# Optimization experiments

Measured on AMD Instinct MI355X. Metric: run time of the kernel, lower is better.

The kernel has to match this reference:

```python
import jax, jax.numpy as jnp
import numpy as np
import math

HIDDEN = 2048
HEADS = 16
HEAD_DIM = HIDDEN // HEADS
MAX_SEQ = 4096
ROPE_BASE = 10000.0


def rope_cos_sin(seq_len):
    # (seq_len, head_dim//2) angle table
    inv_freq = 1.0 / (ROPE_BASE ** (jnp.arange(0, HEAD_DIM, 2, dtype=jnp.float32) / HEAD_DIM))
    t = jnp.arange(seq_len, dtype=jnp.float32)
    ang = jnp.einsum('s,f->sf', t, inv_freq)
    return jnp.cos(ang), jnp.sin(ang)


def apply_rope(x, cos, sin):
    # x: (b, s, h, d); interleaved complex pairs along last dim
    b, s, h, d = x.shape
    xr = x.reshape(b, s, h, d // 2, 2)
    x0, x1 = xr[..., 0], xr[..., 1]
    c = cos[:s][None, :, None, :]
    sn = sin[:s][None, :, None, :]
    o0 = x0 * c - x1 * sn
    o1 = x0 * sn + x1 * c
    return jnp.stack([o0, o1], axis=-1).reshape(b, s, h, d)


def setup_inputs() -> dict:
    key = jax.random.key(0)
    k1, k2, k3, k4, k5, k6 = jax.random.split(key, 6)
    B, SQ, SK = 2, 2048, 2048
    x = jax.random.normal(k1, (B, SQ, HIDDEN), dtype=jnp.float32)
    enc = jax.random.normal(k2, (B, SK, HIDDEN), dtype=jnp.float32)
    mask = jnp.ones((B, SK), dtype=jnp.int32)
    scale = 0.02
    Wq = jax.random.normal(k3, (HIDDEN, HIDDEN), dtype=jnp.float32) * scale
    Wk = jax.random.normal(k4, (HIDDEN, HIDDEN), dtype=jnp.float32) * scale
    Wv = jax.random.normal(k5, (HIDDEN, HIDDEN), dtype=jnp.float32) * scale
    Wo = jax.random.normal(k6, (HIDDEN, HIDDEN), dtype=jnp.float32) * scale
    return {"x": x, "encoder_output": enc, "encoder_attention_mask": mask,
            "Wq": Wq, "Wk": Wk, "Wv": Wv, "Wo": Wo}


def reference(x, encoder_output, encoder_attention_mask, Wq, Wk, Wv, Wo):
    B, SQ, _ = x.shape
    SK = encoder_output.shape[1]
    # nn.Linear(bias=False): y = x @ W^T
    q = (x @ Wq.T).reshape(B, SQ, HEADS, HEAD_DIM)
    k = (encoder_output @ Wk.T).reshape(B, SK, HEADS, HEAD_DIM)
    v = (encoder_output @ Wv.T).reshape(B, SK, HEADS, HEAD_DIM)
    cos, sin = rope_cos_sin(max(SQ, SK))
    q = apply_rope(q, cos, sin)
    k = apply_rope(k, cos, sin)
    scale = math.sqrt(HEAD_DIM)
    # (b, h, sq, sk) scores
    scores = jnp.einsum('bqhd,bkhd->bhqk', q, k) / scale
    mask = encoder_attention_mask[:, None, None, :]
    scores = jnp.where(mask == 0, -jnp.inf, scores)
    attn = jax.nn.softmax(scores, axis=-1)
    out = jnp.einsum('bhqk,bkhd->bqhd', attn, v).reshape(B, SQ, HIDDEN)
    return out @ Wo.T
```

## Files before the change

### kernel.cpp

```cpp
#include <hip/hip_runtime.h>
#include <stdint.h>


#define LOG2E 1.44269504088896340736f
#define INV2PI 0.15915494309189535f

typedef __attribute__((ext_vector_type(8))) short bf16x8;
typedef __attribute__((ext_vector_type(8))) uint16_t u16x8;
typedef __attribute__((ext_vector_type(4))) uint16_t u16x4;
typedef __attribute__((ext_vector_type(4))) float f32x4;

__device__ __forceinline__ uint16_t f2bf(float f) {
  union { float f; uint32_t i; } v; v.f = f;
  uint32_t x = v.i;
  return (uint16_t)((x + 0x7fffu + ((x >> 16) & 1u)) >> 16);
}
__device__ __forceinline__ uint32_t f_as_u(float f) { union { float f; uint32_t u; } v; v.f = f; return v.u; }
__device__ __forceinline__ float u_as_f(uint32_t u) { union { uint32_t u; float f; } v; v.u = u; return v.f; }
__device__ __forceinline__ void glds16(const void* g, void* l) {
  __builtin_amdgcn_global_load_lds((const __attribute__((address_space(1))) void*)g,
                                   (__attribute__((address_space(3))) void*)l, 16, 0, 0);
}

__global__ __launch_bounds__(256) void convert_f32_bf16(const float* __restrict__ in,
                                                        uint16_t* __restrict__ out) {
  const long i = ((long)blockIdx.x * 256 + threadIdx.x) * 8;
  const f32x4 a = *(const f32x4*)(in + i);
  const f32x4 b = *(const f32x4*)(in + i + 4);
  u16x8 o;
#pragma unroll
  for (int j = 0; j < 4; ++j) { o[j] = f2bf(a[j]); o[4 + j] = f2bf(b[j]); }
  *(u16x8*)(out + i) = o;
}

__global__ __launch_bounds__(256) void convert_w4(const float* __restrict__ Wq,
                                                  const float* __restrict__ Wk,
                                                  const float* __restrict__ Wv,
                                                  const float* __restrict__ Wo,
                                                  uint16_t* __restrict__ W4) {
  const int blk = blockIdx.x;
  const int sec = blk >> 11;
  const long off = ((long)(blk & 2047) * 256 + threadIdx.x) * 8;
  const float* src = (sec == 0) ? Wq : (sec == 1) ? Wk : (sec == 2) ? Wv : Wo;
  const f32x4 a = *(const f32x4*)(src + off);
  const f32x4 b = *(const f32x4*)(src + off + 4);
  u16x8 o;
#pragma unroll
  for (int j = 0; j < 4; ++j) { o[j] = f2bf(a[j]); o[4 + j] = f2bf(b[j]); }
  *(u16x8*)(W4 + (long)sec * 4194304 + off) = o;
}

__global__ __launch_bounds__(256) void mask_bias(const int* __restrict__ m,
                                                 float* __restrict__ bias) {
  const int i = blockIdx.x * 256 + threadIdx.x;
  bias[i] = m[i] ? 0.0f : -__builtin_inff();
}

#define EPI_QKV 0
#define EPI_F32 1

__device__ __forceinline__ void epi_rope_store(uint16_t* C, const f32x4& a, int rowbase,
                                               int c, float oscale) {
  const int f = (c >> 1) & 63;
  const float inv = __builtin_amdgcn_exp2f((float)f * (-13.287712379549449f / 64.0f));
  const float sgn = (c & 1) ? 1.0f : -1.0f;
#pragma unroll
  for (int r = 0; r < 4; ++r) {
    const float val = a[r];
    const float partner = __shfl_xor(val, 1);
    const int s = (rowbase + r) & 2047;
    const float rev = __builtin_amdgcn_fractf((float)s * inv * INV2PI);
    const float sn = __builtin_amdgcn_sinf(rev);
    const float cs = __builtin_amdgcn_cosf(rev);
    C[(long)(rowbase + r) * 2048 + c] = f2bf((val * cs + sgn * partner * sn) * oscale);
  }
}

template <int MODE>
__global__ __launch_bounds__(512, 2) void gemm256(const uint16_t* __restrict__ A0,
                                                  const uint16_t* __restrict__ A1,
                                                  const uint16_t* __restrict__ W,
                                                  void* __restrict__ C0v,
                                                  void* __restrict__ C1v,
                                                  void* __restrict__ C2v,
                                                  int M, int N, int K, float oscale) {
  __shared__ __align__(16) uint16_t As[2][2][8192];
  __shared__ __align__(16) uint16_t Bs[2][2][8192];
  const int tid = threadIdx.x;
  const int lane = tid & 63;
  const int w = tid >> 6;
  const int r16 = lane & 15, quad = lane >> 4;
  const int wm = w >> 2, wn = w & 3;

  const int nby = M >> 8;
  const int nwg = gridDim.x;
  const int wg = ((int)blockIdx.x & 7) * (nwg >> 3) + ((int)blockIdx.x >> 3);
  const int by = wg % nby, bx = wg / nby;
  const int m0 = by << 8, n0 = bx << 8;

  const uint16_t* A = (MODE == EPI_QKV && n0 >= 2048) ? A1 : A0;

  const int srow = 2 * w * 16 + (lane >> 2);
  const int ssl = (lane & 3) ^ ((srow >> 1) & 3);
  const uint16_t* Ag0 = A + (long)(m0 + srow) * K + ssl * 8;
  const uint16_t* Ag1 = Ag0 + (long)16 * K;
  const uint16_t* Bg0 = W + (long)(n0 + srow) * K + ssl * 8;
  const uint16_t* Bg1 = Bg0 + (long)16 * K;
  const int ldso = w << 10;

  const int sw = (r16 >> 1) & 3;
  const int aoff = (wm * 128 + r16) * 32 + ((quad ^ sw) << 3);
  const int boff = (wn * 64 + r16) * 32 + ((quad ^ sw) << 3);

  f32x4 acc[8][4] = {};
  bf16x8 af[4], bfr[4];

#define SCHED0() __builtin_amdgcn_sched_barrier(0)
#define G_STAGE_A(BUF, KK, T) do { \
    glds16(Ag0 + (long)(T) * 64 + (KK) * 32, &As[BUF][KK][ldso]); \
    glds16(Ag1 + (long)(T) * 64 + (KK) * 32, &As[BUF][KK][ldso + 512]); } while (0)
#define G_STAGE_B(BUF, KK, T) do { \
    glds16(Bg0 + (long)(T) * 64 + (KK) * 32, &Bs[BUF][KK][ldso]); \
    glds16(Bg1 + (long)(T) * 64 + (KK) * 32, &Bs[BUF][KK][ldso + 512]); } while (0)
#define LDS_B(BUF, KK) do { _Pragma("unroll") \
    for (int i = 0; i < 4; ++i) bfr[i] = *(const bf16x8*)&Bs[BUF][KK][boff + i * 512]; } while (0)
#define LDS_A(BUF, KK, MH) do { _Pragma("unroll") \
    for (int i = 0; i < 4; ++i) af[i] = *(const bf16x8*)&As[BUF][KK][aoff + ((MH) * 4 + i) * 512]; } while (0)
#define MFMA16(MH) do { __builtin_amdgcn_s_setprio(1); _Pragma("unroll") \
    for (int mi = 0; mi < 4; ++mi) { _Pragma("unroll") \
      for (int nt = 0; nt < 4; ++nt) \
        acc[(MH) * 4 + mi][nt] = __builtin_amdgcn_mfma_f32_16x16x32_bf16(af[mi], bfr[nt], acc[(MH) * 4 + mi][nt], 0, 0, 0); } \
    __builtin_amdgcn_s_setprio(0); } while (0)
#define VMBAR(NN) do { SCHED0(); \
    asm volatile("s_waitcnt vmcnt(" #NN ")" ::: "memory"); \
    __builtin_amdgcn_s_barrier(); \
    SCHED0(); } while (0)
#define TILE_ITER(T, BC, BN) do { \
    G_STAGE_A(BN, 0, (T) + 1); LDS_B(BC, 0); LDS_A(BC, 0, 0); MFMA16(0); \
    G_STAGE_B(BN, 0, (T) + 1); LDS_A(BC, 0, 1); MFMA16(1); \
    VMBAR(4); \
    G_STAGE_A(BN, 1, (T) + 1); LDS_B(BC, 1); LDS_A(BC, 1, 0); MFMA16(0); \
    G_STAGE_B(BN, 1, (T) + 1); LDS_A(BC, 1, 1); MFMA16(1); \
    VMBAR(4); } while (0)

  G_STAGE_A(0, 0, 0); G_STAGE_B(0, 0, 0); G_STAGE_A(0, 1, 0); G_STAGE_B(0, 1, 0);
  VMBAR(4);

  const int NT = K >> 6;
  int t = 0;
  for (; t + 2 < NT; t += 2) { TILE_ITER(t, 0, 1); TILE_ITER(t + 1, 1, 0); }
  TILE_ITER(t, 0, 1);

  LDS_B(1, 0); LDS_A(1, 0, 0); MFMA16(0);
  LDS_A(1, 0, 1); MFMA16(1);
  VMBAR(0);
  LDS_B(1, 1); LDS_A(1, 1, 0); MFMA16(0);
  LDS_A(1, 1, 1); MFMA16(1);

#undef SCHED0
#undef G_STAGE_A
#undef G_STAGE_B
#undef LDS_A
#undef LDS_B
#undef MFMA16
#undef VMBAR
#undef TILE_ITER

#pragma unroll
  for (int mt = 0; mt < 8; ++mt)
#pragma unroll
    for (int nt = 0; nt < 4; ++nt) {
      const int col = n0 + wn * 64 + nt * 16 + r16;
      const int rowbase = m0 + wm * 128 + mt * 16 + quad * 4;
      if constexpr (MODE == EPI_F32) {
        float* C = (float*)C0v;
#pragma unroll
        for (int r = 0; r < 4; ++r)
          C[(long)(rowbase + r) * N + col] = acc[mt][nt][r];
      } else {
        if (n0 < 2048) {
          epi_rope_store((uint16_t*)C0v, acc[mt][nt], rowbase, col, oscale);
        } else if (n0 < 4096) {
          epi_rope_store((uint16_t*)C1v, acc[mt][nt], rowbase, col - 2048, 1.0f);
        } else {
          uint16_t* Vt = (uint16_t*)C2v;
          const int c = col - 4096;
          const int h = c >> 7, d = c & 127;
          const int b = rowbase >> 11, s = rowbase & 2047;
          u16x4 pk;
#pragma unroll
          for (int r = 0; r < 4; ++r) pk[r] = f2bf(acc[mt][nt][r]);
          *(u16x4*)(Vt + (long)((b * 16 + h) * 128 + d) * 2048 + s) = pk;
        }
      }
    }
}

__global__ __launch_bounds__(256) void attn_kernel(const uint16_t* __restrict__ Q,
                                                   const uint16_t* __restrict__ K,
                                                   const uint16_t* __restrict__ Vt,
                                                   const float* __restrict__ bias,
                                                   uint16_t* __restrict__ O) {
  __shared__ __align__(16) uint16_t Ks[2][32 * 128];
  __shared__ __align__(16) uint16_t Vts[2][128 * 32];
  __shared__ __align__(16) uint16_t Ps[4][32 * 40];
  const int tid = threadIdx.x;
  const int lane = tid & 63;
  const int w = tid >> 6;
  const int r16 = lane & 15, quad = lane >> 4;
  const int h = blockIdx.y, b = blockIdx.z;
  const int qbase = blockIdx.x * 128 + w * 32;

  bf16x8 qf[2][4];
#pragma unroll
  for (int t = 0; t < 2; ++t) {
    const uint16_t* qb = Q + ((long)(b * 2048 + qbase + t * 16 + r16)) * 2048 + h * 128 + quad * 8;
#pragma unroll
    for (int c = 0; c < 4; ++c) qf[t][c] = *(const bf16x8*)(qb + c * 32);
  }
  f32x4 oacc[2][8] = {};
  float li[2][4] = {};

  uint16_t* PsW = &Ps[w][0];
  const float* brow = bias + b * 2048;

  const int key0[2] = {8 * w + quad, 8 * w + 4 + quad};
  const uint16_t* kg[2];
  const uint16_t* vg[2];
#pragma unroll
  for (int i = 0; i < 2; ++i) {
    kg[i] = K + ((long)(b * 2048 + key0[i])) * 2048 + h * 128 + 8 * (r16 ^ ((4 * i + quad) & 7));
    const int dim = 32 * w + 16 * i + (lane >> 2);
    vg[i] = Vt + ((long)((b * 16 + h) * 128 + dim)) * 2048 + 8 * ((lane & 3) ^ ((lane >> 2) & 3));
  }

#pragma unroll
  for (int i = 0; i < 2; ++i) {
    glds16(kg[i], &Ks[0][(2 * w + i) * 512]);
    glds16(vg[i], &Vts[0][(2 * w + i) * 512]);
    kg[i] += 32 * 2048;
    vg[i] += 32;
  }
  float bn0 = brow[r16], bn1 = brow[16 + r16];

  auto body = [&](int k0, const uint16_t* Kc, const uint16_t* Vc,
                  uint16_t* Kn, uint16_t* Vn, bool pf) {
    __syncthreads();
    const float bc0 = bn0, bc1 = bn1;
    if (pf) {
#pragma unroll
      for (int i = 0; i < 2; ++i) {
        glds16(kg[i], Kn + (2 * w + i) * 512);
        glds16(vg[i], Vn + (2 * w + i) * 512);
        kg[i] += 32 * 2048;
        vg[i] += 32;
      }
      bn0 = brow[k0 + 32 + r16];
      bn1 = brow[k0 + 48 + r16];
    }
#pragma unroll
    for (int ct = 0; ct < 2; ++ct) {
      const int key = ct * 16 + r16;
      const int kb = key & 7;
      bf16x8 kf[4];
#pragma unroll
      for (int c = 0; c < 4; ++c)
        kf[c] = *(const bf16x8*)(Kc + key * 128 + ((4 * c + quad) ^ kb) * 8);
      const float bv = ct ? bc1 : bc0;
      const int pc = ct * 2 + (r16 >> 3);
#pragma unroll
      for (int t = 0; t < 2; ++t) {
        f32x4 s = {};
#pragma unroll
        for (int c = 0; c < 4; ++c)
          s = __builtin_amdgcn_mfma_f32_16x16x32_bf16(qf[t][c], kf[c], s, 0, 0, 0);
#pragma unroll
        for (int r = 0; r < 4; ++r) {
          const float p = __builtin_amdgcn_exp2f(s[r] + bv);
          const uint32_t pb = f_as_u(p) + 0x8000u;
          const int row = t * 16 + quad * 4 + r;
          PsW[row * 40 + ((pc ^ r) << 3) + (r16 & 7)] = (uint16_t)(pb >> 16);
          li[t][r] += u_as_f(pb & 0xffff0000u);
        }
      }
    }
    bf16x8 pa[2];
#pragma unroll
    for (int t = 0; t < 2; ++t)
      pa[t] = *(const bf16x8*)(PsW + (t * 16 + r16) * 40 + ((quad ^ (r16 & 3)) << 3));
#pragma unroll
    for (int nt = 0; nt < 8; ++nt) {
      const int dim = nt * 16 + r16;
      bf16x8 vf = *(const bf16x8*)(Vc + dim * 32 + ((quad ^ (dim & 3)) << 3));
#pragma unroll
      for (int t = 0; t < 2; ++t)
        oacc[t][nt] = __builtin_amdgcn_mfma_f32_16x16x32_bf16(pa[t], vf, oacc[t][nt], 0, 0, 0);
    }
  };

  for (int kt2 = 0; kt2 < 32; ++kt2) {
    body(64 * kt2,      &Ks[0][0], &Vts[0][0], &Ks[1][0], &Vts[1][0], true);
    body(64 * kt2 + 32, &Ks[1][0], &Vts[1][0], &Ks[0][0], &Vts[0][0], kt2 < 31);
  }

#pragma unroll
  for (int off = 1; off < 16; off <<= 1)
#pragma unroll
    for (int t = 0; t < 2; ++t)
#pragma unroll
      for (int r = 0; r < 4; ++r) li[t][r] += __shfl_xor(li[t][r], off);

#pragma unroll
  for (int t = 0; t < 2; ++t) {
    uint16_t* ob = O + ((long)(b * 2048 + qbase + t * 16)) * 2048 + h * 128;
    float inv_l[4];
#pragma unroll
    for (int r = 0; r < 4; ++r) inv_l[r] = 1.0f / li[t][r];
#pragma unroll
    for (int nt = 0; nt < 8; ++nt)
#pragma unroll
      for (int r = 0; r < 4; ++r)
        ob[(long)(quad * 4 + r) * 2048 + nt * 16 + r16] = f2bf(oacc[t][nt][r] * inv_l[r]);
  }
}

extern "C" void kernel_launch(void* const* d_in, const int* in_sizes, int n_in,
                              void* d_out, int out_size, void* d_ws, size_t ws_size,
                              hipStream_t stream) {
  const float* x   = (const float*)d_in[0];
  const float* enc = (const float*)d_in[1];
  const int*   msk = (const int*)d_in[2];
  const float* Wq  = (const float*)d_in[3];
  const float* Wk  = (const float*)d_in[4];
  const float* Wv  = (const float*)d_in[5];
  const float* Wo  = (const float*)d_in[6];
  float* out = (float*)d_out;

  const long NELT = 8L * 1024 * 1024;
  const long WELT = 4L * 1024 * 1024;
  uint16_t* Qb  = (uint16_t*)d_ws;
  uint16_t* Kb  = Qb + NELT;
  uint16_t* Vtb = Kb + NELT;
  uint16_t* W4  = Vtb + NELT;
  float* biasb  = (float*)(W4 + 4 * WELT);
  uint16_t* xb   = (uint16_t*)d_out;
  uint16_t* encb = xb + NELT;
  uint16_t* Ob   = W4;

  const float cs_exp = 0.088388347648318447f * LOG2E;

  convert_f32_bf16<<<(int)(NELT / 2048), 256, 0, stream>>>(x, xb);
  convert_f32_bf16<<<(int)(NELT / 2048), 256, 0, stream>>>(enc, encb);
  convert_w4<<<8192, 256, 0, stream>>>(Wq, Wk, Wv, Wo, W4);
  mask_bias<<<16, 256, 0, stream>>>(msk, biasb);

  gemm256<EPI_QKV><<<384, 512, 0, stream>>>(xb, encb, W4, Qb, Kb, Vtb,
                                            4096, 6144, 2048, cs_exp);

  attn_kernel<<<dim3(16, 16, 2), 256, 0, stream>>>(Qb, Kb, Vtb, biasb, Ob);

  gemm256<EPI_F32><<<128, 512, 0, stream>>>(Ob, nullptr, W4 + 3 * WELT,
                                            out, nullptr, nullptr,
                                            4096, 2048, 2048, 1.0f);
}
```

Baseline: 461.2 us.

## Restructure GEMM main loop into barrier-separated load and MFMA phases

Reorganizes the bf16 GEMM inner loop so each half-tile issues its LDS reads and global-to-LDS prefetch first, then waits on a workgroup barrier and lgkmcnt(0) before its MFMA block, with an extra barrier after each MFMA phase. The intent is a ping-pong-style schedule where waves alternate memory and matrix phases in lockstep, reducing contention between LDS traffic and MFMA issue. It adds four extra barriers per tile and forces full LDS waits, which could serialize work that previously overlapped.

```diff
diff --git a/kernel.cpp b/kernel.cpp
--- a/kernel.cpp
+++ b/kernel.cpp
@@ -131,31 +131,36 @@
       for (int nt = 0; nt < 4; ++nt) \
         acc[(MH) * 4 + mi][nt] = __builtin_amdgcn_mfma_f32_16x16x32_bf16(af[mi], bfr[nt], acc[(MH) * 4 + mi][nt], 0, 0, 0); } \
     __builtin_amdgcn_s_setprio(0); } while (0)
-#define VMBAR(NN) do { SCHED0(); \
+#define PH_MFMA(MH) do { SCHED0(); __builtin_amdgcn_s_barrier(); \
+    asm volatile("s_waitcnt lgkmcnt(0)" ::: "memory"); SCHED0(); \
+    MFMA16(MH); } while (0)
+#define PH_END() do { SCHED0(); __builtin_amdgcn_s_barrier(); SCHED0(); } while (0)
+#define PH_END_VM(NN) do { SCHED0(); \
     asm volatile("s_waitcnt vmcnt(" #NN ")" ::: "memory"); \
-    __builtin_amdgcn_s_barrier(); \
-    SCHED0(); } while (0)
-#define TILE_ITER(T, BC, BN) do { \
-    G_STAGE_A(BN, 0, (T) + 1); LDS_B(BC, 0); LDS_A(BC, 0, 0); MFMA16(0); \
-    G_STAGE_B(BN, 0, (T) + 1); LDS_A(BC, 0, 1); MFMA16(1); \
-    VMBAR(4); \
-    G_STAGE_A(BN, 1, (T) + 1); LDS_B(BC, 1); LDS_A(BC, 1, 0); MFMA16(0); \
-    G_STAGE_B(BN, 1, (T) + 1); LDS_A(BC, 1, 1); MFMA16(1); \
-    VMBAR(4); } while (0)
+    __builtin_amdgcn_s_barrier(); SCHED0(); } while (0)
+
+#define TILE_MAIN(T, BC, BN) do { \
+    LDS_B(BC, 0); LDS_A(BC, 0, 0); G_STAGE_A(BN, 0, (T) + 1); \
+    PH_MFMA(0); PH_END(); \
+    LDS_A(BC, 0, 1); G_STAGE_B(BN, 0, (T) + 1); \
+    PH_MFMA(1); PH_END_VM(4); \
+    LDS_B(BC, 1); LDS_A(BC, 1, 0); G_STAGE_A(BN, 1, (T) + 1); \
+    PH_MFMA(0); PH_END(); \
+    LDS_A(BC, 1, 1); G_STAGE_B(BN, 1, (T) + 1); \
+    PH_MFMA(1); PH_END_VM(4); } while (0)
 
   G_STAGE_A(0, 0, 0); G_STAGE_B(0, 0, 0); G_STAGE_A(0, 1, 0); G_STAGE_B(0, 1, 0);
-  VMBAR(4);
+  PH_END_VM(4);
 
   const int NT = K >> 6;
   int t = 0;
-  for (; t + 2 < NT; t += 2) { TILE_ITER(t, 0, 1); TILE_ITER(t + 1, 1, 0); }
-  TILE_ITER(t, 0, 1);
-
-  LDS_B(1, 0); LDS_A(1, 0, 0); MFMA16(0);
-  LDS_A(1, 0, 1); MFMA16(1);
-  VMBAR(0);
-  LDS_B(1, 1); LDS_A(1, 1, 0); MFMA16(0);
-  LDS_A(1, 1, 1); MFMA16(1);
+  for (; t < NT - 2; t += 2) { TILE_MAIN(t, 0, 1); TILE_MAIN(t + 1, 1, 0); }
+  TILE_MAIN(t, 0, 1);
+
+  LDS_B(1, 0); LDS_A(1, 0, 0); PH_MFMA(0); PH_END();
+  LDS_A(1, 0, 1);              PH_MFMA(1); PH_END_VM(0);
+  LDS_B(1, 1); LDS_A(1, 1, 0); PH_MFMA(0); PH_END();
+  LDS_A(1, 1, 1);              PH_MFMA(1);
 
 #undef SCHED0
 #undef G_STAGE_A
@@ -163,8 +168,10 @@
 #undef LDS_A
 #undef LDS_B
 #undef MFMA16
-#undef VMBAR
-#undef TILE_ITER
+#undef PH_MFMA
+#undef PH_END
+#undef PH_END_VM
+#undef TILE_MAIN
 
 #pragma unroll
   for (int mt = 0; mt < 8; ++mt)
```

New measurement: 467.0 us. Within noise of the previous version (+1.2%).

## Add 128x256-tile output projection GEMM to double workgroup count

Applied to the files above, without the earlier changes.

Replaces the templated 256x256-tile GEMM used for the output projection with a dedicated kernel that uses 128x256 tiles, so the 4096x2048 projection launches 256 workgroups instead of 128. Each wave now holds a 4x4 accumulator block, and the A staging buffer is halved. The goal is to fill more compute units on the chip, since 128 workgroups leave many idle. The cost is lower per-tile data reuse and more redundant B-tile loads. The QKV GEMM loses its template parameter but otherwise computes the same thing.

```diff
diff --git a/kernel.cpp b/kernel.cpp
--- a/kernel.cpp
+++ b/kernel.cpp
@@ -56,9 +56,6 @@
   bias[i] = m[i] ? 0.0f : -__builtin_inff();
 }
 
-#define EPI_QKV 0
-#define EPI_F32 1
-
 __device__ __forceinline__ void epi_rope_store(uint16_t* C, const f32x4& a, int rowbase,
                                                int c, float oscale) {
   const int f = (c >> 1) & 63;
@@ -76,13 +73,12 @@
   }
 }
 
-template <int MODE>
 __global__ __launch_bounds__(512, 2) void gemm256(const uint16_t* __restrict__ A0,
                                                   const uint16_t* __restrict__ A1,
                                                   const uint16_t* __restrict__ W,
-                                                  void* __restrict__ C0v,
-                                                  void* __restrict__ C1v,
-                                                  void* __restrict__ C2v,
+                                                  uint16_t* __restrict__ Qb,
+                                                  uint16_t* __restrict__ Kb,
+                                                  uint16_t* __restrict__ Vtb,
                                                   int M, int N, int K, float oscale) {
   __shared__ __align__(16) uint16_t As[2][2][8192];
   __shared__ __align__(16) uint16_t Bs[2][2][8192];
@@ -98,7 +94,7 @@
   const int by = wg % nby, bx = wg / nby;
   const int m0 = by << 8, n0 = bx << 8;
 
-  const uint16_t* A = (MODE == EPI_QKV && n0 >= 2048) ? A1 : A0;
+  const uint16_t* A = (n0 >= 2048) ? A1 : A0;
 
   const int srow = 2 * w * 16 + (lane >> 2);
   const int ssl = (lane & 3) ^ ((srow >> 1) & 3);
@@ -157,13 +153,10 @@
   LDS_B(1, 1); LDS_A(1, 1, 0); MFMA16(0);
   LDS_A(1, 1, 1); MFMA16(1);
 
-#undef SCHED0
 #undef G_STAGE_A
 #undef G_STAGE_B
 #undef LDS_A
 #undef LDS_B
-#undef MFMA16
-#undef VMBAR
 #undef TILE_ITER
 
 #pragma unroll
@@ -172,27 +165,107 @@
     for (int nt = 0; nt < 4; ++nt) {
       const int col = n0 + wn * 64 + nt * 16 + r16;
       const int rowbase = m0 + wm * 128 + mt * 16 + quad * 4;
-      if constexpr (MODE == EPI_F32) {
-        float* C = (float*)C0v;
-#pragma unroll
-        for (int r = 0; r < 4; ++r)
-          C[(long)(rowbase + r) * N + col] = acc[mt][nt][r];
+      if (n0 < 2048) {
+        epi_rope_store(Qb, acc[mt][nt], rowbase, col, oscale);
+      } else if (n0 < 4096) {
+        epi_rope_store(Kb, acc[mt][nt], rowbase, col - 2048, 1.0f);
       } else {
-        if (n0 < 2048) {
-          epi_rope_store((uint16_t*)C0v, acc[mt][nt], rowbase, col, oscale);
-        } else if (n0 < 4096) {
-          epi_rope_store((uint16_t*)C1v, acc[mt][nt], rowbase, col - 2048, 1.0f);
-        } else {
-          uint16_t* Vt = (uint16_t*)C2v;
-          const int c = col - 4096;
-          const int h = c >> 7, d = c & 127;
-          const int b = rowbase >> 11, s = rowbase & 2047;
-          u16x4 pk;
-#pragma unroll
-          for (int r = 0; r < 4; ++r) pk[r] = f2bf(acc[mt][nt][r]);
-          *(u16x4*)(Vt + (long)((b * 16 + h) * 128 + d) * 2048 + s) = pk;
-        }
+        const int c = col - 4096;
+        const int h = c >> 7, d = c & 127;
+        const int b = rowbase >> 11, s = rowbase & 2047;
+        u16x4 pk;
+#pragma unroll
+        for (int r = 0; r < 4; ++r) pk[r] = f2bf(acc[mt][nt][r]);
+        *(u16x4*)(Vtb + (long)((b * 16 + h) * 128 + d) * 2048 + s) = pk;
       }
+    }
+}
+
+__global__ __launch_bounds__(512, 2) void gemm_proj(const uint16_t* __restrict__ A0,
+                                                    const uint16_t* __restrict__ W,
+                                                    float* __restrict__ C,
+                                                    int M, int N, int K) {
+  __shared__ __align__(16) uint16_t As[2][2][4096];
+  __shared__ __align__(16) uint16_t Bs[2][2][8192];
+  const int tid = threadIdx.x;
+  const int lane = tid & 63;
+  const int w = tid >> 6;
+  const int r16 = lane & 15, quad = lane >> 4;
+  const int wm = w >> 2, wn = w & 3;
+
+  const int nby = M >> 7;
+  const int nwg = gridDim.x;
+  const int wg = ((int)blockIdx.x & 7) * (nwg >> 3) + ((int)blockIdx.x >> 3);
+  const int by = wg % nby, bx = wg / nby;
+  const int m0 = by << 7, n0 = bx << 8;
+
+  const int sa_row = 16 * w + (lane >> 2);
+  const int sb_row = 32 * w + (lane >> 2);
+  const int ssl = (lane & 3) ^ (((lane >> 2) >> 1) & 3);
+  const uint16_t* Ag = A0 + (long)(m0 + sa_row) * K + ssl * 8;
+  const uint16_t* Bg0 = W + (long)(n0 + sb_row) * K + ssl * 8;
+  const uint16_t* Bg1 = Bg0 + (long)16 * K;
+
+  const int sw = (r16 >> 1) & 3;
+  const int aoff = (wm * 64 + r16) * 32 + ((quad ^ sw) << 3);
+  const int boff = (wn * 64 + r16) * 32 + ((quad ^ sw) << 3);
+
+  f32x4 acc[4][4] = {};
+  bf16x8 af[4], bfr[4];
+
+#define PG_STAGE_A(BUF, KK, T) \
+    glds16(Ag + (long)(T) * 64 + (KK) * 32, &As[BUF][KK][w * 512])
+#define PG_STAGE_B(BUF, KK, T) do { \
+    glds16(Bg0 + (long)(T) * 64 + (KK) * 32, &Bs[BUF][KK][2 * w * 512]); \
+    glds16(Bg1 + (long)(T) * 64 + (KK) * 32, &Bs[BUF][KK][2 * w * 512 + 512]); } while (0)
+#define PLDS_B(BUF, KK) do { _Pragma("unroll") \
+    for (int i = 0; i < 4; ++i) bfr[i] = *(const bf16x8*)&Bs[BUF][KK][boff + i * 512]; } while (0)
+#define PLDS_A(BUF, KK) do { _Pragma("unroll") \
+    for (int i = 0; i < 4; ++i) af[i] = *(const bf16x8*)&As[BUF][KK][aoff + i * 512]; } while (0)
+#define PMFMA(MT0, MT1) do { __builtin_amdgcn_s_setprio(1); _Pragma("unroll") \
+    for (int mi = (MT0); mi < (MT1); ++mi) { _Pragma("unroll") \
+      for (int nt = 0; nt < 4; ++nt) \
+        acc[mi][nt] = __builtin_amdgcn_mfma_f32_16x16x32_bf16(af[mi], bfr[nt], acc[mi][nt], 0, 0, 0); } \
+    __builtin_amdgcn_s_setprio(0); } while (0)
+#define PTILE(T, BC, BN) do { \
+    PG_STAGE_A(BN, 0, (T) + 1); PLDS_B(BC, 0); PLDS_A(BC, 0); PMFMA(0, 2); \
+    PG_STAGE_B(BN, 0, (T) + 1); PMFMA(2, 4); \
+    VMBAR(3); \
+    PG_STAGE_A(BN, 1, (T) + 1); PLDS_B(BC, 1); PLDS_A(BC, 1); PMFMA(0, 2); \
+    PG_STAGE_B(BN, 1, (T) + 1); PMFMA(2, 4); \
+    VMBAR(3); } while (0)
+
+  PG_STAGE_A(0, 0, 0); PG_STAGE_B(0, 0, 0); PG_STAGE_A(0, 1, 0); PG_STAGE_B(0, 1, 0);
+  VMBAR(3);
+
+  const int NT = K >> 6;
+  int t = 0;
+  for (; t + 2 < NT; t += 2) { PTILE(t, 0, 1); PTILE(t + 1, 1, 0); }
+  PTILE(t, 0, 1);
+
+  PLDS_B(1, 0); PLDS_A(1, 0); PMFMA(0, 4);
+  VMBAR(0);
+  PLDS_B(1, 1); PLDS_A(1, 1); PMFMA(0, 4);
+
+#undef PG_STAGE_A
+#undef PG_STAGE_B
+#undef PLDS_A
+#undef PLDS_B
+#undef PMFMA
+#undef PTILE
+#undef MFMA16
+#undef VMBAR
+#undef SCHED0
+
+#pragma unroll
+  for (int mt = 0; mt < 4; ++mt)
+#pragma unroll
+    for (int nt = 0; nt < 4; ++nt) {
+      const int col = n0 + wn * 64 + nt * 16 + r16;
+      const int rowbase = m0 + wm * 64 + mt * 16 + quad * 4;
+#pragma unroll
+      for (int r = 0; r < 4; ++r)
+        C[(long)(rowbase + r) * N + col] = acc[mt][nt][r];
     }
 }
 
@@ -354,12 +427,10 @@
   convert_w4<<<8192, 256, 0, stream>>>(Wq, Wk, Wv, Wo, W4);
   mask_bias<<<16, 256, 0, stream>>>(msk, biasb);
 
-  gemm256<EPI_QKV><<<384, 512, 0, stream>>>(xb, encb, W4, Qb, Kb, Vtb,
-                                            4096, 6144, 2048, cs_exp);
+  gemm256<<<384, 512, 0, stream>>>(xb, encb, W4, Qb, Kb, Vtb,
+                                   4096, 6144, 2048, cs_exp);
 
   attn_kernel<<<dim3(16, 16, 2), 256, 0, stream>>>(Qb, Kb, Vtb, biasb, Ob);
 
-  gemm256<EPI_F32><<<128, 512, 0, stream>>>(Ob, nullptr, W4 + 3 * WELT,
-                                            out, nullptr, nullptr,
-                                            4096, 2048, 2048, 1.0f);
-}
+  gemm_proj<<<256, 512, 0, stream>>>(Ob, W4 + 3 * WELT, out, 4096, 2048, 2048);
+}
```

Result: faster. 446.0 us (-3.3%).
